# Optimization experiments

Hardware: AMD Instinct MI355X
Metric: run time of the kernel (lower is better)

## Reference

```python
import jax, jax.numpy as jnp
import numpy as np

WH, WW = 14, 14
N_TOK = WH * WW + 1  # 197 (CLS + patches)
NUM_HEADS = 16
HEAD_DIM = 64
SCALE = HEAD_DIM ** -0.5
NUM_REL = (2 * WH - 1) * (2 * WW - 1) + 3  # 732
LN_EPS = 1e-5


def _make_rel_pos_index():
    coords = np.stack(np.meshgrid(np.arange(WH), np.arange(WW), indexing='ij'))  # [2,Wh,Ww]
    flat = coords.reshape(2, -1)                          # [2, Wh*Ww]
    rel = flat[:, :, None] - flat[:, None, :]             # [2, P, P]
    rel = rel.transpose(1, 2, 0).copy()                   # [P, P, 2]
    rel[:, :, 0] += WH - 1
    rel[:, :, 1] += WW - 1
    rel[:, :, 0] *= 2 * WW - 1
    idx = np.zeros((N_TOK, N_TOK), dtype=np.int32)
    idx[1:, 1:] = rel.sum(-1)
    idx[0, 0:] = NUM_REL - 3
    idx[0:, 0] = NUM_REL - 2
    idx[0, 0] = NUM_REL - 1
    return jnp.asarray(idx)

REL_POS_INDEX = _make_rel_pos_index()  # [197,197] int32 constant


def _layer_norm(x, g, b):
    mu = jnp.mean(x, axis=-1, keepdims=True)
    var = jnp.var(x, axis=-1, keepdims=True)
    return (x - mu) * jax.lax.rsqrt(var + LN_EPS) * g + b


def setup_inputs() -> dict:
    key = jax.random.key(0)
    ks = jax.random.split(key, 12)
    D, H = 1024, 4096
    s = lambda d: 1.0 / np.sqrt(d)
    return {
        'x': jax.random.normal(ks[0], (64, N_TOK, D), jnp.float32),
        'qkv_w': jax.random.normal(ks[1], (3 * D, D), jnp.float32) * s(D),
        'q_bias': jax.random.normal(ks[2], (D,), jnp.float32) * 0.02,
        'v_bias': jax.random.normal(ks[3], (D,), jnp.float32) * 0.02,
        'rel_bias_table': jax.random.normal(ks[4], (NUM_REL, NUM_HEADS), jnp.float32) * 0.02,
        'proj_w': jax.random.normal(ks[5], (D, D), jnp.float32) * s(D),
        'proj_b': jax.random.normal(ks[6], (D,), jnp.float32) * 0.02,
        'ln1_g': jnp.ones((D,), jnp.float32),
        'ln1_b': jnp.zeros((D,), jnp.float32),
        'ln2_g': jnp.ones((D,), jnp.float32),
        'ln2_b': jnp.zeros((D,), jnp.float32),
        'fc1_w': jax.random.normal(ks[7], (H, D), jnp.float32) * s(D),
        'fc1_b': jax.random.normal(ks[8], (H,), jnp.float32) * 0.02,
        'fc2_w': jax.random.normal(ks[9], (D, H), jnp.float32) * s(H),
        'fc2_b': jax.random.normal(ks[10], (D,), jnp.float32) * 0.02,
    }


def reference(x, qkv_w, q_bias, v_bias, rel_bias_table, proj_w, proj_b,
              ln1_g, ln1_b, ln2_g, ln2_b, fc1_w, fc1_b, fc2_w, fc2_b):
    B, N, C = x.shape
    # --- attention branch ---
    h = _layer_norm(x, ln1_g, ln1_b)
    qkv_b = jnp.concatenate([q_bias, jnp.zeros_like(v_bias), v_bias])
    qkv = h @ qkv_w.T + qkv_b                                 # [B,N,3C]
    qkv = qkv.reshape(B, N, 3, NUM_HEADS, HEAD_DIM).transpose(2, 0, 3, 1, 4)
    q, k, v = qkv[0], qkv[1], qkv[2]                          # [B,H,N,hd]
    attn = jnp.einsum('bhqd,bhkd->bhqk', q * SCALE, k)        # [B,H,N,N]
    rel_bias = rel_bias_table[REL_POS_INDEX]                  # [N,N,H]
    attn = attn + rel_bias.transpose(2, 0, 1)[None]           # gathered bias add
    attn = jax.nn.softmax(attn, axis=-1)
    o = jnp.einsum('bhqk,bhkd->bhqd', attn, v)                # [B,H,N,hd]
    o = o.transpose(0, 2, 1, 3).reshape(B, N, C)
    o = o @ proj_w.T + proj_b
    x = x + o
    # --- MLP branch ---
    h2 = _layer_norm(x, ln2_g, ln2_b)
    h2 = jax.nn.gelu(h2 @ fc1_w.T + fc1_b, approximate=False)
    h2 = h2 @ fc2_w.T + fc2_b
    return x + h2
```

## Files before the change

### kernel.cpp

```cpp
#include <hip/hip_runtime.h>
#include <hip/hip_bf16.h>
#include <cstdint>

typedef __attribute__((ext_vector_type(8))) short bf16x8;
typedef __attribute__((ext_vector_type(4))) float f32x4;

#define AS1 __attribute__((address_space(1)))
#define AS3 __attribute__((address_space(3)))

__device__ __forceinline__ void gload16(const void* g, void* l) {
  __builtin_amdgcn_global_load_lds((const AS1 unsigned int*)g,
                                   (AS3 unsigned int*)l, 16, 0, 0);
}

__device__ __forceinline__ unsigned short f2bf(float f) {
  unsigned int u = __builtin_bit_cast(unsigned int, f);
  u += 0x7FFFu + ((u >> 16) & 1u);
  return (unsigned short)(u >> 16);
}

__device__ __forceinline__ float fast_gelu(float x) {
  float z = fabsf(x) * 0.70710678118654752f;
  float t = __builtin_amdgcn_rcpf(1.0f + 0.3275911f * z);
  float poly = t * (0.254829592f + t * (-0.284496736f + t * (1.421413741f +
               t * (-1.453152027f + t * 1.061405429f))));
  float erf_abs = 1.0f - poly * __expf(-z * z);
  float erfv = (x < 0.0f) ? -erf_abs : erf_abs;
  return 0.5f * x * (1.0f + erfv);
}

__global__ __launch_bounds__(256) void cvt_all(
    const float* __restrict__ s0, unsigned short* __restrict__ d0, int n0,
    const float* __restrict__ s1, unsigned short* __restrict__ d1, int n1,
    const float* __restrict__ s2, unsigned short* __restrict__ d2, int n2,
    const float* __restrict__ s3, unsigned short* __restrict__ d3, int n3) {
  int total = n0 + n1 + n2 + n3;
  int stride = gridDim.x * 256;
  for (int i = blockIdx.x * 256 + threadIdx.x; i < total; i += stride) {
    const float* s; unsigned short* d; int j = i;
    if (j < n0) { s = s0; d = d0; }
    else if ((j -= n0) < n1) { s = s1; d = d1; }
    else if ((j -= n1) < n2) { s = s2; d = d2; }
    else { j -= n2; s = s3; d = d3; }
    float4 v = ((const float4*)s)[j];
    ushort4 st;
    st.x = f2bf(v.x); st.y = f2bf(v.y); st.z = f2bf(v.z); st.w = f2bf(v.w);
    ((ushort4*)d)[j] = st;
  }
}

__global__ __launch_bounds__(256) void ln_kernel(const float* __restrict__ x,
                                                 const float* __restrict__ gw,
                                                 const float* __restrict__ bw,
                                                 unsigned short* __restrict__ out,
                                                 int rows) {
  int row = blockIdx.x;
  if (row >= rows) return;
  const float4* xr = (const float4*)(x + (size_t)row * 1024);
  int tid = threadIdx.x;
  float4 v = xr[tid];
  float s = v.x + v.y + v.z + v.w;
  float s2 = v.x * v.x + v.y * v.y + v.z * v.z + v.w * v.w;
  #pragma unroll
  for (int m = 1; m < 64; m <<= 1) { s += __shfl_xor(s, m); s2 += __shfl_xor(s2, m); }
  __shared__ float ls[4], ls2[4];
  int wv = tid >> 6;
  if ((tid & 63) == 0) { ls[wv] = s; ls2[wv] = s2; }
  __syncthreads();
  s = ls[0] + ls[1] + ls[2] + ls[3];
  s2 = ls2[0] + ls2[1] + ls2[2] + ls2[3];
  float mu = s * (1.0f / 1024.0f);
  float var = s2 * (1.0f / 1024.0f) - mu * mu;
  float rs = rsqrtf(var + 1e-5f);
  float4 g4 = ((const float4*)gw)[tid];
  float4 b4 = ((const float4*)bw)[tid];
  ushort4 st;
  st.x = f2bf((v.x - mu) * rs * g4.x + b4.x);
  st.y = f2bf((v.y - mu) * rs * g4.y + b4.y);
  st.z = f2bf((v.z - mu) * rs * g4.z + b4.z);
  st.w = f2bf((v.w - mu) * rs * g4.w + b4.w);
  ((ushort4*)(out + (size_t)row * 1024))[tid] = st;
}

#define QUAD(MI0, NI0, AF)                                                    \
    __builtin_amdgcn_s_setprio(1);                                            \
    _Pragma("unroll")                                                         \
    for (int mi = 0; mi < 4; ++mi)                                            \
      _Pragma("unroll")                                                       \
      for (int ni = 0; ni < 2; ++ni) {                                        \
        acc[MI0 + mi][NI0 + ni] = __builtin_amdgcn_mfma_f32_16x16x32_bf16(    \
            AF[mi][0], bfrag[NI0 + ni][0], acc[MI0 + mi][NI0 + ni], 0, 0, 0); \
        acc[MI0 + mi][NI0 + ni] = __builtin_amdgcn_mfma_f32_16x16x32_bf16(    \
            AF[mi][1], bfrag[NI0 + ni][1], acc[MI0 + mi][NI0 + ni], 0, 0, 0); \
      }                                                                       \
    __builtin_amdgcn_s_setprio(0);

template<int EPI>
__global__ __launch_bounds__(512) void gemm8(
    const unsigned short* __restrict__ A, const unsigned short* __restrict__ B,
    int M, int N, int K, int CP,
    const float* __restrict__ bias0, const float* __restrict__ bias1,
    const float* __restrict__ resid,
    unsigned short* __restrict__ o0, unsigned short* __restrict__ o1,
    unsigned short* __restrict__ o2, float* __restrict__ f_out) {
  extern __shared__ unsigned short smem[];
  const int tid = threadIdx.x;
  const int lane = tid & 63;
  const int wid = tid >> 6;
  const int wr = wid >> 2;
  const int wc = wid & 3;
  const int lane15 = lane & 15, l16 = lane >> 4;

  const int nwg = gridDim.x;
  const int bid = blockIdx.x;
  const int q = nwg >> 3, rmd = nwg & 7;
  const int xcd = bid & 7, idx = bid >> 3;
  const int sb = (xcd < rmd ? xcd * (q + 1) : rmd * (q + 1) + (xcd - rmd) * q) + idx;
  const int brow = sb / CP, bcol = sb - brow * CP;
  const long row0 = (long)brow * 256;
  const long col0 = (long)bcol * 256;
  const int NT = K >> 6;

  unsigned short* Alds = smem;
  unsigned short* Blds = smem + 32768;

  const int srow8 = tid >> 3;
  const int sg8 = (((tid & 7) ^ (srow8 & 7)) << 3);
  auto stageHalf = [&](const unsigned short* src, long gr0, long kofs,
                       unsigned short* dst) {
    gload16(src + (gr0 + srow8) * (long)K + kofs + sg8, dst + (size_t)tid * 8);
    gload16(src + (gr0 + 64 + srow8) * (long)K + kofs + sg8,
            dst + 4096 + (size_t)tid * 8);
  };

  const int browB = (wc & 1) * 64;
  const int slx = lane15 & 7;
  auto ldsA = [&](const unsigned short* base, int mi, int kk) -> bf16x8 {
    const int r = mi * 16 + lane15;
    const int sl = ((kk << 2) | l16) ^ slx;
    return *(const bf16x8*)(base + r * 64 + sl * 8);
  };
  auto ldsB = [&](const unsigned short* base, int ni, int kk) -> bf16x8 {
    const int r = browB + ni * 16 + lane15;
    const int sl = ((kk << 2) | l16) ^ slx;
    return *(const bf16x8*)(base + r * 64 + sl * 8);
  };

  f32x4 acc[8][4] = {};

  stageHalf(B, col0,       0, Blds);
  stageHalf(B, col0 + 128, 0, Blds + 8192);
  stageHalf(A, row0,       0, Alds);
  stageHalf(A, row0 + 128, 0, Alds + 8192);
  if (NT > 1) {
    stageHalf(B, col0,       64, Blds + 16384);
    stageHalf(B, col0 + 128, 64, Blds + 16384 + 8192);
    asm volatile("s_waitcnt vmcnt(4)" ::: "memory");
  } else {
    asm volatile("s_waitcnt vmcnt(0)" ::: "memory");
  }
  __builtin_amdgcn_s_barrier();

  for (int t = 0; t < NT; ++t) {
    const int buf = t & 1;
    const unsigned short* Ab = Alds + buf * 16384 + wr * 8192;
    const unsigned short* Bb = Blds + buf * 16384 + (wc >> 1) * 8192;
    unsigned short* Anext  = Alds + (buf ^ 1) * 16384;
    unsigned short* Bnext2 = Blds + buf * 16384;
    const long k1 = (long)(t + 1) << 6;
    const long k2 = (long)(t + 2) << 6;

    bf16x8 bfrag[4][2], afU[4][2], afL[4][2];

    #pragma unroll
    for (int mi = 0; mi < 4; ++mi) {
      afU[mi][0] = ldsA(Ab, mi, 0);
      afU[mi][1] = ldsA(Ab, mi, 1);
    }
    #pragma unroll
    for (int ni = 0; ni < 2; ++ni) {
      bfrag[ni][0] = ldsB(Bb, ni, 0);
      bfrag[ni][1] = ldsB(Bb, ni, 1);
    }
    if (t + 1 < NT) stageHalf(A, row0, k1, Anext);
    __builtin_amdgcn_s_barrier();
    asm volatile("s_waitcnt lgkmcnt(0)" ::: "memory");
    __builtin_amdgcn_sched_barrier(0);
    QUAD(0, 0, afU)
    __builtin_amdgcn_s_barrier();

    #pragma unroll
    for (int ni = 2; ni < 4; ++ni) {
      bfrag[ni][0] = ldsB(Bb, ni, 0);
      bfrag[ni][1] = ldsB(Bb, ni, 1);
    }
    if (t + 1 < NT) stageHalf(A, row0 + 128, k1, Anext + 8192);
    __builtin_amdgcn_s_barrier();
    asm volatile("s_waitcnt lgkmcnt(0)" ::: "memory");
    __builtin_amdgcn_sched_barrier(0);
    QUAD(0, 2, afU)
    __builtin_amdgcn_s_barrier();

    #pragma unroll
    for (int mi = 0; mi < 4; ++mi) {
      afL[mi][0] = ldsA(Ab, mi + 4, 0);
      afL[mi][1] = ldsA(Ab, mi + 4, 1);
    }
    if (t + 2 < NT) stageHalf(B, col0, k2, Bnext2);
    __builtin_amdgcn_s_barrier();
    asm volatile("s_waitcnt lgkmcnt(0)" ::: "memory");
    __builtin_amdgcn_sched_barrier(0);
    QUAD(4, 0, afL)
    __builtin_amdgcn_s_barrier();

    if (t + 2 < NT) stageHalf(B, col0 + 128, k2, Bnext2 + 8192);
    __builtin_amdgcn_s_barrier();
    QUAD(4, 2, afL)
    if (t + 2 < NT)      { asm volatile("s_waitcnt vmcnt(4)" ::: "memory"); }
    else if (t + 1 < NT) { asm volatile("s_waitcnt vmcnt(0)" ::: "memory"); }
    if (t + 1 < NT) __builtin_amdgcn_s_barrier();
  }

  const int lrow = l16 * 4;
  if constexpr (EPI == 0) {
    const int colbase = (int)col0 + wc * 64;
    const int part = colbase >> 10;
    const int hd0 = colbase & 1023;
    const int head = hd0 >> 6;
    unsigned short* dst = (part == 0) ? o0 : (part == 1 ? o1 : o2);
    const float scl = (part == 0) ? 0.125f : 1.0f;
    float bias[4];
    #pragma unroll
    for (int ni = 0; ni < 4; ++ni) {
      int hd = hd0 + ni * 16 + lane15;
      bias[ni] = (part == 0) ? bias0[hd] : (part == 2 ? bias1[hd] : 0.0f);
    }
    #pragma unroll
    for (int mi = 0; mi < 8; ++mi) {
      #pragma unroll
      for (int r = 0; r < 4; ++r) {
        int irow = (int)row0 + wr * 128 + mi * 16 + lrow + r;
        if (irow >= M) continue;
        int bb = irow / 197, tk = irow - bb * 197;
        long obase = ((long)(bb * 16 + head) * 197 + tk) * 64;
        #pragma unroll
        for (int ni = 0; ni < 4; ++ni)
          dst[obase + ni * 16 + lane15] = f2bf((acc[mi][ni][r] + bias[ni]) * scl);
      }
    }
  } else {
    float bias[4];
    #pragma unroll
    for (int ni = 0; ni < 4; ++ni)
      bias[ni] = bias0[col0 + wc * 64 + ni * 16 + lane15];
    #pragma unroll
    for (int mi = 0; mi < 8; ++mi) {
      #pragma unroll
      for (int r = 0; r < 4; ++r) {
        long row = row0 + wr * 128 + mi * 16 + lrow + r;
        if (row >= M) continue;
        long cbase = col0 + wc * 64 + lane15;
        #pragma unroll
        for (int ni = 0; ni < 4; ++ni) {
          long col = cbase + ni * 16;
          float cv = acc[mi][ni][r] + bias[ni];
          if constexpr (EPI == 2) {
            o0[row * (long)N + col] = f2bf(fast_gelu(cv));
          } else {
            f_out[row * 1024 + col] = cv + resid[row * 1024 + col];
          }
        }
      }
    }
  }
}

__device__ __forceinline__ int relidx(int q, int k) {
  if (q == 0) return (k == 0) ? 731 : 729;
  if (k == 0) return 730;
  int qp = q - 1, kp = k - 1;
  int qi = qp / 14, qj = qp - qi * 14;
  int ki = kp / 14, kj = kp - ki * 14;
  return (qi - ki + 13) * 27 + (qj - kj + 13);
}

__global__ __launch_bounds__(256) void build_bias(const float* __restrict__ rel_tab,
                                                  unsigned short* __restrict__ bt) {
  int kk = threadIdx.x;
  if (kk >= 224) return;
  int qq = blockIdx.x;
  int head = blockIdx.y;
  unsigned short v = 0;
  if (qq < 197 && kk < 197)
    v = f2bf(rel_tab[relidx(qq, kk) * 16 + head]);
  bt[((long)head * 208 + qq) * 224 + kk] = v;
}

__global__ __launch_bounds__(256) void attn_kernel(
    const unsigned short* __restrict__ qg, const unsigned short* __restrict__ kg,
    const unsigned short* __restrict__ vg, const unsigned short* __restrict__ bias_tab,
    unsigned short* __restrict__ og) {
  __shared__ __align__(16) unsigned short Vt[64][224];
  __shared__ __align__(16) unsigned short Ps[4][16][224];

  const int tid = threadIdx.x;
  const int bh = blockIdx.x;
  const int head = bh & 15;
  const int b = bh >> 4;
  const unsigned short* qp = qg + (long)bh * 197 * 64;
  const unsigned short* kp = kg + (long)bh * 197 * 64;
  const unsigned short* vp = vg + (long)bh * 197 * 64;
  const unsigned short* bt = bias_tab + (long)head * 208 * 224;

  {
    ushort4 z; z.x = 0; z.y = 0; z.z = 0; z.w = 0;
    for (int i = tid; i < 64 * 8; i += 256) {
      int row = i >> 3, j = i & 7;
      ((ushort4*)&Vt[row][192])[j] = z;
    }
    for (int i = tid; i < 4 * 16 * 4; i += 256) {
      int w = i >> 6, rr = (i >> 2) & 15, j = i & 3;
      ((ushort4*)&Ps[w][rr][208])[j] = z;
    }
  }
  __syncthreads();
  for (int i = tid; i < 197 * 8; i += 256) {
    int row = i >> 3, c8 = (i & 7) * 8;
    bf16x8 vv = *(const bf16x8*)(vp + row * 64 + c8);
    #pragma unroll
    for (int j = 0; j < 8; ++j) Vt[c8 + j][row] = (unsigned short)vv[j];
  }
  __syncthreads();

  const int wv = tid >> 6, lane = tid & 63;
  const int lcol = lane & 15;
  const int lk8 = (lane >> 4) * 8;
  const int lrow4 = (lane >> 4) * 4;

  for (int strip = wv; strip < 13; strip += 4) {
    bf16x8 aq[2];
    #pragma unroll
    for (int kk = 0; kk < 2; ++kk)
      aq[kk] = *(const bf16x8*)(qp + (strip * 16 + lcol) * 64 + kk * 32 + lk8);
    f32x4 s[13];
    #pragma unroll
    for (int kt = 0; kt < 13; ++kt) {
      f32x4 z = {};
      #pragma unroll
      for (int kk = 0; kk < 2; ++kk) {
        bf16x8 bk = *(const bf16x8*)(kp + (kt * 16 + lcol) * 64 + kk * 32 + lk8);
        z = __builtin_amdgcn_mfma_f32_16x16x32_bf16(aq[kk], bk, z, 0, 0, 0);
      }
      s[kt] = z;
    }
    #pragma unroll
    for (int kt = 0; kt < 13; ++kt) {
      int ktok = kt * 16 + lcol;
      if (ktok >= 197) {
        #pragma unroll
        for (int r = 0; r < 4; ++r) s[kt][r] = -1e30f;
      } else {
        #pragma unroll
        for (int r = 0; r < 4; ++r) {
          int qq = strip * 16 + lrow4 + r;
          unsigned int bu = bt[qq * 224 + ktok];
          s[kt][r] += __builtin_bit_cast(float, bu << 16);
        }
      }
    }
    #pragma unroll
    for (int r = 0; r < 4; ++r) {
      float m = s[0][r];
      #pragma unroll
      for (int kt = 1; kt < 13; ++kt) m = fmaxf(m, s[kt][r]);
      #pragma unroll
      for (int d = 1; d < 16; d <<= 1) m = fmaxf(m, __shfl_xor(m, d));
      float sum = 0.0f;
      #pragma unroll
      for (int kt = 0; kt < 13; ++kt) { float p = __expf(s[kt][r] - m); s[kt][r] = p; sum += p; }
      #pragma unroll
      for (int d = 1; d < 16; d <<= 1) sum += __shfl_xor(sum, d);
      float rinv = 1.0f / sum;
      #pragma unroll
      for (int kt = 0; kt < 13; ++kt) s[kt][r] *= rinv;
    }
    #pragma unroll
    for (int kt = 0; kt < 13; ++kt)
      #pragma unroll
      for (int r = 0; r < 4; ++r)
        Ps[wv][lrow4 + r][kt * 16 + lcol] = f2bf(s[kt][r]);
    #pragma unroll
    for (int dt = 0; dt < 4; ++dt) {
      f32x4 oacc = {};
      #pragma unroll
      for (int kc = 0; kc < 7; ++kc) {
        bf16x8 ap = *(const bf16x8*)(&Ps[wv][lcol][kc * 32 + lk8]);
        bf16x8 bv = *(const bf16x8*)(&Vt[dt * 16 + lcol][kc * 32 + lk8]);
        oacc = __builtin_amdgcn_mfma_f32_16x16x32_bf16(ap, bv, oacc, 0, 0, 0);
      }
      #pragma unroll
      for (int r = 0; r < 4; ++r) {
        int qq = strip * 16 + lrow4 + r;
        if (qq < 197)
          og[((long)b * 197 + qq) * 1024 + head * 64 + dt * 16 + lcol] = f2bf(oacc[r]);
      }
    }
  }
}

extern "C" void kernel_launch(void* const* d_in, const int* in_sizes, int n_in,
                              void* d_out, int out_size, void* d_ws, size_t ws_size,
                              hipStream_t stream) {
  const float* x        = (const float*)d_in[0];
  const float* qkv_w    = (const float*)d_in[1];
  const float* q_bias   = (const float*)d_in[2];
  const float* v_bias   = (const float*)d_in[3];
  const float* rel_tab  = (const float*)d_in[4];
  const float* proj_w   = (const float*)d_in[5];
  const float* proj_b   = (const float*)d_in[6];
  const float* ln1_g    = (const float*)d_in[7];
  const float* ln1_b    = (const float*)d_in[8];
  const float* ln2_g    = (const float*)d_in[9];
  const float* ln2_b    = (const float*)d_in[10];
  const float* fc1_w    = (const float*)d_in[11];
  const float* fc1_b    = (const float*)d_in[12];
  const float* fc2_w    = (const float*)d_in[13];
  const float* fc2_b    = (const float*)d_in[14];
  float* out = (float*)d_out;
  char* ws = (char*)d_ws;

  const int M = 64 * 197;
  const size_t MP = 12800;
  const int RB = 50;

  size_t off = 0;
  auto take = [&](size_t bytes) { size_t o = off; off += (bytes + 255) & ~(size_t)255; return o; };
  size_t o_wqkv = take((size_t)3072 * 1024 * 2);
  size_t o_wproj = take((size_t)1024 * 1024 * 2);
  size_t o_wfc1 = take((size_t)4096 * 1024 * 2);
  size_t o_wfc2 = take((size_t)1024 * 4096 * 2);
  size_t o_big  = take(MP * 4096 * 2);
  size_t o_o    = take(MP * 1024 * 2);
  size_t o_bias = take((size_t)16 * 208 * 224 * 2);

  unsigned short* wqkv = (unsigned short*)(ws + o_wqkv);
  unsigned short* wproj = (unsigned short*)(ws + o_wproj);
  unsigned short* wfc1 = (unsigned short*)(ws + o_wfc1);
  unsigned short* wfc2 = (unsigned short*)(ws + o_wfc2);
  unsigned short* h   = (unsigned short*)(ws + o_big);
  unsigned short* qb  = (unsigned short*)(ws + o_big + MP * 1024 * 2);
  unsigned short* kb  = qb + (size_t)64 * 16 * 197 * 64;
  unsigned short* vb  = kb + (size_t)64 * 16 * 197 * 64;
  unsigned short* g   = (unsigned short*)(ws + o_big);
  unsigned short* ob  = (unsigned short*)(ws + o_o);
  unsigned short* h2  = ob;
  unsigned short* btab = (unsigned short*)(ws + o_bias);
  float* x1 = out;

  cvt_all<<<2048, 256, 0, stream>>>(qkv_w, wqkv, 3145728 / 4,
                                    proj_w, wproj, 1048576 / 4,
                                    fc1_w, wfc1, 4194304 / 4,
                                    fc2_w, wfc2, 4194304 / 4);

  build_bias<<<dim3(208, 16), 256, 0, stream>>>(rel_tab, btab);

  ln_kernel<<<M, 256, 0, stream>>>(x, ln1_g, ln1_b, h, M);

  gemm8<0><<<RB * 12, 512, 131072, stream>>>(h, wqkv, M, 3072, 1024, 12,
      q_bias, v_bias, nullptr, qb, kb, vb, nullptr);

  attn_kernel<<<1024, 256, 0, stream>>>(qb, kb, vb, btab, ob);

  gemm8<1><<<RB * 4, 512, 131072, stream>>>(ob, wproj, M, 1024, 1024, 4,
      proj_b, nullptr, x, nullptr, nullptr, nullptr, x1);

  ln_kernel<<<M, 256, 0, stream>>>(x1, ln2_g, ln2_b, h2, M);

  gemm8<2><<<RB * 16, 512, 131072, stream>>>(h2, wfc1, M, 4096, 1024, 16,
      fc1_b, nullptr, nullptr, g, nullptr, nullptr, nullptr);

  gemm8<3><<<RB * 4, 512, 131072, stream>>>(g, wfc2, M, 1024, 4096, 4,
      fc2_b, nullptr, x1, nullptr, nullptr, nullptr, out);
}
```

Measured before the change: 573.0 us.

## Software-pipeline LDS fragment loads across GEMM iterations and cut barriers

Restructures the bf16 MFMA GEMM main loop so LDS fragment reads for the next quadrant, and for the next k-tile, are issued before the current MFMA quadrant runs. Partial lgkmcnt waits replace full drains, and the number of workgroup barriers per k-iteration drops from about seven to two. The aim is to hide LDS latency behind MFMA work and cut synchronisation stalls. The cost is more live fragment registers, which could reduce occupancy, plus subtle ordering hazards between the async global->LDS stages and the reads.

```diff
diff --git a/kernel.cpp b/kernel.cpp
--- a/kernel.cpp
+++ b/kernel.cpp
@@ -82,16 +82,16 @@
   ((ushort4*)(out + (size_t)row * 1024))[tid] = st;
 }
 
-#define QUAD(MI0, NI0, AF)                                                    \
+#define QUAD(MI0, NI0, AF, BF)                                                \
     __builtin_amdgcn_s_setprio(1);                                            \
     _Pragma("unroll")                                                         \
     for (int mi = 0; mi < 4; ++mi)                                            \
       _Pragma("unroll")                                                       \
       for (int ni = 0; ni < 2; ++ni) {                                        \
         acc[MI0 + mi][NI0 + ni] = __builtin_amdgcn_mfma_f32_16x16x32_bf16(    \
-            AF[mi][0], bfrag[NI0 + ni][0], acc[MI0 + mi][NI0 + ni], 0, 0, 0); \
+            AF[mi][0], BF[ni][0], acc[MI0 + mi][NI0 + ni], 0, 0, 0);          \
         acc[MI0 + mi][NI0 + ni] = __builtin_amdgcn_mfma_f32_16x16x32_bf16(    \
-            AF[mi][1], bfrag[NI0 + ni][1], acc[MI0 + mi][NI0 + ni], 0, 0, 0); \
+            AF[mi][1], BF[ni][1], acc[MI0 + mi][NI0 + ni], 0, 0, 0);          \
       }                                                                       \
     __builtin_amdgcn_s_setprio(0);
 
@@ -147,6 +147,7 @@
   };
 
   f32x4 acc[8][4] = {};
+  bf16x8 afU[4][2], afL[4][2], b01[2][2], b23[2][2];
 
   stageHalf(B, col0,       0, Blds);
   stageHalf(B, col0 + 128, 0, Blds + 8192);
@@ -160,65 +161,73 @@
     asm volatile("s_waitcnt vmcnt(0)" ::: "memory");
   }
   __builtin_amdgcn_s_barrier();
+  __builtin_amdgcn_sched_barrier(0);
+  {
+    const unsigned short* Ab0 = Alds + wr * 8192;
+    const unsigned short* Bb0 = Blds + (wc >> 1) * 8192;
+    #pragma unroll
+    for (int mi = 0; mi < 4; ++mi) {
+      afU[mi][0] = ldsA(Ab0, mi, 0); afU[mi][1] = ldsA(Ab0, mi, 1);
+    }
+    #pragma unroll
+    for (int ni = 0; ni < 2; ++ni) {
+      b01[ni][0] = ldsB(Bb0, ni, 0); b01[ni][1] = ldsB(Bb0, ni, 1);
+    }
+  }
 
   for (int t = 0; t < NT; ++t) {
     const int buf = t & 1;
-    const unsigned short* Ab = Alds + buf * 16384 + wr * 8192;
-    const unsigned short* Bb = Blds + buf * 16384 + (wc >> 1) * 8192;
+    const unsigned short* AbC = Alds + buf * 16384 + wr * 8192;
+    const unsigned short* BbC = Blds + buf * 16384 + (wc >> 1) * 8192;
+    const unsigned short* AbN = Alds + (buf ^ 1) * 16384 + wr * 8192;
+    const unsigned short* BbN = Blds + (buf ^ 1) * 16384 + (wc >> 1) * 8192;
     unsigned short* Anext  = Alds + (buf ^ 1) * 16384;
     unsigned short* Bnext2 = Blds + buf * 16384;
     const long k1 = (long)(t + 1) << 6;
     const long k2 = (long)(t + 2) << 6;
 
-    bf16x8 bfrag[4][2], afU[4][2], afL[4][2];
+    #pragma unroll
+    for (int ni = 0; ni < 2; ++ni) {
+      b23[ni][0] = ldsB(BbC, ni + 2, 0); b23[ni][1] = ldsB(BbC, ni + 2, 1);
+    }
+    if (t + 1 < NT) stageHalf(A, row0, k1, Anext);
+    asm volatile("s_waitcnt lgkmcnt(4)" ::: "memory");
+    __builtin_amdgcn_sched_barrier(0);
+    QUAD(0, 0, afU, b01)
 
     #pragma unroll
     for (int mi = 0; mi < 4; ++mi) {
-      afU[mi][0] = ldsA(Ab, mi, 0);
-      afU[mi][1] = ldsA(Ab, mi, 1);
-    }
-    #pragma unroll
-    for (int ni = 0; ni < 2; ++ni) {
-      bfrag[ni][0] = ldsB(Bb, ni, 0);
-      bfrag[ni][1] = ldsB(Bb, ni, 1);
-    }
-    if (t + 1 < NT) stageHalf(A, row0, k1, Anext);
+      afL[mi][0] = ldsA(AbC, mi + 4, 0); afL[mi][1] = ldsA(AbC, mi + 4, 1);
+    }
+    if (t + 1 < NT) stageHalf(A, row0 + 128, k1, Anext + 8192);
+    asm volatile("s_waitcnt lgkmcnt(8)" ::: "memory");
+    __builtin_amdgcn_sched_barrier(0);
+    QUAD(0, 2, afU, b23)
+
     __builtin_amdgcn_s_barrier();
+    __builtin_amdgcn_sched_barrier(0);
+    if (t + 2 < NT) stageHalf(B, col0, k2, Bnext2);
     asm volatile("s_waitcnt lgkmcnt(0)" ::: "memory");
     __builtin_amdgcn_sched_barrier(0);
-    QUAD(0, 0, afU)
-    __builtin_amdgcn_s_barrier();
-
-    #pragma unroll
-    for (int ni = 2; ni < 4; ++ni) {
-      bfrag[ni][0] = ldsB(Bb, ni, 0);
-      bfrag[ni][1] = ldsB(Bb, ni, 1);
-    }
-    if (t + 1 < NT) stageHalf(A, row0 + 128, k1, Anext + 8192);
-    __builtin_amdgcn_s_barrier();
-    asm volatile("s_waitcnt lgkmcnt(0)" ::: "memory");
-    __builtin_amdgcn_sched_barrier(0);
-    QUAD(0, 2, afU)
-    __builtin_amdgcn_s_barrier();
-
-    #pragma unroll
-    for (int mi = 0; mi < 4; ++mi) {
-      afL[mi][0] = ldsA(Ab, mi + 4, 0);
-      afL[mi][1] = ldsA(Ab, mi + 4, 1);
-    }
-    if (t + 2 < NT) stageHalf(B, col0, k2, Bnext2);
-    __builtin_amdgcn_s_barrier();
-    asm volatile("s_waitcnt lgkmcnt(0)" ::: "memory");
-    __builtin_amdgcn_sched_barrier(0);
-    QUAD(4, 0, afL)
-    __builtin_amdgcn_s_barrier();
+    QUAD(4, 0, afL, b01)
 
     if (t + 2 < NT) stageHalf(B, col0 + 128, k2, Bnext2 + 8192);
-    __builtin_amdgcn_s_barrier();
-    QUAD(4, 2, afL)
-    if (t + 2 < NT)      { asm volatile("s_waitcnt vmcnt(4)" ::: "memory"); }
-    else if (t + 1 < NT) { asm volatile("s_waitcnt vmcnt(0)" ::: "memory"); }
-    if (t + 1 < NT) __builtin_amdgcn_s_barrier();
+    if (t + 1 < NT) {
+      if (t + 2 < NT) { asm volatile("s_waitcnt vmcnt(4)" ::: "memory"); }
+      else            { asm volatile("s_waitcnt vmcnt(0)" ::: "memory"); }
+      __builtin_amdgcn_s_barrier();
+      __builtin_amdgcn_sched_barrier(0);
+      #pragma unroll
+      for (int mi = 0; mi < 4; ++mi) {
+        afU[mi][0] = ldsA(AbN, mi, 0); afU[mi][1] = ldsA(AbN, mi, 1);
+      }
+      #pragma unroll
+      for (int ni = 0; ni < 2; ++ni) {
+        b01[ni][0] = ldsB(BbN, ni, 0); b01[ni][1] = ldsB(BbN, ni, 1);
+      }
+      __builtin_amdgcn_sched_barrier(0);
+    }
+    QUAD(4, 2, afL, b23)
   }
 
   const int lrow = l16 * 4;
```

Measured after the change: 592.8 us. 1.03x slower.
